# Kernel optimization log

Hardware: AMD Instinct MI355X
Metric: run time of the kernel (lower is better)

The kernel has to match this reference:

```python
import jax, jax.numpy as jnp
import numpy as np

L = 2          # num_layers
B = 64         # batch
T = 256        # seq len (== max_len)
I = 1024       # input_size
H = 1024       # hidden_size
G = 2 * H      # gate size
EPS = 1e-5


def setup_inputs() -> dict:
    key = jax.random.key(0)
    ks = jax.random.split(key, 12)
    stdv = 1.0 / np.sqrt(H)
    u = lambda k, shp: jax.random.uniform(k, shp, jnp.float32, -stdv, stdv)
    return {
        "x": jax.random.normal(ks[0], (B, T, I), jnp.float32),
        "hx": jax.random.normal(ks[1], (L, B, H), jnp.float32),
        "w_ih": u(ks[2], (L, G, I)),
        "w_hh": u(ks[3], (L, G, H)),
        "b_ih": u(ks[4], (L, G)),
        "b_hh": u(ks[5], (L, G)),
        # SeparatedBatchNorm1d affine params: weight ~ U[0,1], bias = 0 (per reset_parameters)
        "bn_i_w": jax.random.uniform(ks[6], (L, G), jnp.float32),
        "bn_i_b": jnp.zeros((L, G), jnp.float32),
        "bn_h_w": jax.random.uniform(ks[7], (L, G), jnp.float32),
        "bn_h_b": jnp.zeros((L, G), jnp.float32),
    }


def _bn(v, w, b):
    # training-mode batch norm over the batch dim (biased variance), affine
    m = jnp.mean(v, axis=0)
    var = jnp.var(v, axis=0)
    return (v - m) * jax.lax.rsqrt(var + EPS) * w + b


def reference(x, hx, w_ih, w_hh, b_ih, b_hh, bn_i_w, bn_i_b, bn_h_w, bn_h_b):
    out = x  # [B, T, I]
    for layer in range(L):
        wih, whh = w_ih[layer], w_hh[layer]
        bih, bhh = b_ih[layer], b_hh[layer]
        iw, ib = bn_i_w[layer], bn_i_b[layer]
        hw, hb = bn_h_w[layer], bn_h_b[layer]

        # precompute input projections + per-step BN outside the recurrence
        def step(h, x_t):
            in_part = _bn(x_t @ wih.T + bih, iw, ib)          # [B, 2H]
            h_part = _bn(h @ whh.T + bhh, hw, hb)             # [B, 2H]
            gates = in_part + h_part
            ug = jax.nn.sigmoid(gates[:, :H])
            og = jax.nn.relu(gates[:, H:])
            h_new = ug * h + (1.0 - ug) * og
            return h_new, h_new

        _, ys = jax.lax.scan(step, hx[layer], jnp.swapaxes(out, 0, 1))  # ys: [T, B, H]
        out = jnp.swapaxes(ys, 0, 1)  # [B, T, H]
    return out
```

## Files before the change

kernel.cpp:

```cpp
#include <hip/hip_runtime.h>
#include <hip/hip_bf16.h>


typedef __attribute__((ext_vector_type(8))) short bf16x8;
typedef __attribute__((ext_vector_type(4))) float f32x4;

__device__ __forceinline__ float wave_sum(float v) {
#pragma unroll
  for (int m = 1; m < 64; m <<= 1) v += __shfl_xor(v, m, 64);
  return v;
}

__device__ __forceinline__ unsigned short f2bf(float f) {
  __hip_bfloat16 h = __float2bfloat16(f);
  return __builtin_bit_cast(unsigned short, h);
}
__device__ __forceinline__ float bf2f(unsigned short u) {
  unsigned int x = ((unsigned int)u) << 16;
  return __builtin_bit_cast(float, x);
}
__device__ __forceinline__ void split2(float v, unsigned short& hi, unsigned short& lo) {
  hi = f2bf(v);
  lo = f2bf(v - bf2f(hi));
}

__global__ __launch_bounds__(256) void wconv(
    const float* __restrict__ w, unsigned short* __restrict__ wh, unsigned short* __restrict__ wl)
{
  int i = ((blockIdx.x << 8) + threadIdx.x) << 3;
#pragma unroll
  for (int j = 0; j < 8; j += 4) {
    float4 a = *(const float4*)(w + i + j);
    ushort4 h, l;
    split2(a.x, h.x, l.x); split2(a.y, h.y, l.y);
    split2(a.z, h.z, l.z); split2(a.w, h.w, l.w);
    *(ushort4*)(wh + i + j) = h;
    *(ushort4*)(wl + i + j) = l;
  }
}

__global__ __launch_bounds__(256) void hinit(
    const float* __restrict__ hx0, unsigned short* __restrict__ hh, unsigned short* __restrict__ hl)
{
  int i = ((blockIdx.x << 8) + threadIdx.x) << 3;
#pragma unroll
  for (int j = 0; j < 8; j += 4) {
    float4 a = *(const float4*)(hx0 + i + j);
    ushort4 h, l;
    split2(a.x, h.x, l.x); split2(a.y, h.y, l.y);
    split2(a.z, h.z, l.z); split2(a.w, h.w, l.w);
    *(ushort4*)(hh + i + j) = h;
    *(ushort4*)(hl + i + j) = l;
  }
}

__global__ __launch_bounds__(256) void proj_gemm(
    const float* __restrict__ in, const float* __restrict__ w,
    float* __restrict__ P, int t0)
{
  __shared__ float As[8][132];
  __shared__ float Bs[8][132];
  const int tid = threadIdx.x;
  const int m0 = blockIdx.y << 7;
  const int n0 = blockIdx.x << 7;
  const int tm = tid >> 4, tn = tid & 15;
  const int lr = tid >> 1;
  const int lk = (tid & 1) << 2;
  const int mA = m0 + lr;
  const int bb = mA & 63;
  const int tg = t0 + (mA >> 6);
  const float* arow = in + ((size_t)bb << 18) + ((size_t)tg << 10) + lk;
  const float* brow = w + ((size_t)(n0 + lr) << 10) + lk;
  float acc[2][2][4][4] = {};
  for (int k0 = 0; k0 < 1024; k0 += 8) {
    float4 av = *(const float4*)(arow + k0);
    float4 bv = *(const float4*)(brow + k0);
    __syncthreads();
    As[lk + 0][lr] = av.x; As[lk + 1][lr] = av.y; As[lk + 2][lr] = av.z; As[lk + 3][lr] = av.w;
    Bs[lk + 0][lr] = bv.x; Bs[lk + 1][lr] = bv.y; Bs[lk + 2][lr] = bv.z; Bs[lk + 3][lr] = bv.w;
    __syncthreads();
#pragma unroll
    for (int kk = 0; kk < 8; ++kk) {
      float4 a0 = *(const float4*)&As[kk][tm << 2];
      float4 a1 = *(const float4*)&As[kk][(tm << 2) + 64];
      float4 b0 = *(const float4*)&Bs[kk][tn << 2];
      float4 b1 = *(const float4*)&Bs[kk][(tn << 2) + 64];
      const float* ap0 = (const float*)&a0;
      const float* ap1 = (const float*)&a1;
      const float* bp0 = (const float*)&b0;
      const float* bp1 = (const float*)&b1;
#pragma unroll
      for (int i = 0; i < 4; ++i)
#pragma unroll
        for (int j = 0; j < 4; ++j) {
          acc[0][0][i][j] = fmaf(ap0[i], bp0[j], acc[0][0][i][j]);
          acc[0][1][i][j] = fmaf(ap0[i], bp1[j], acc[0][1][i][j]);
          acc[1][0][i][j] = fmaf(ap1[i], bp0[j], acc[1][0][i][j]);
          acc[1][1][i][j] = fmaf(ap1[i], bp1[j], acc[1][1][i][j]);
        }
    }
  }
#pragma unroll
  for (int mi = 0; mi < 2; ++mi)
#pragma unroll
    for (int i = 0; i < 4; ++i) {
      int m = m0 + (mi << 6) + (tm << 2) + i;
      float* prow = P + ((size_t)m << 11) + n0 + (tn << 2);
      *(float4*)prow        = make_float4(acc[mi][0][i][0], acc[mi][0][i][1], acc[mi][0][i][2], acc[mi][0][i][3]);
      *(float4*)(prow + 64) = make_float4(acc[mi][1][i][0], acc[mi][1][i][1], acc[mi][1][i][2], acc[mi][1][i][3]);
    }
}

__global__ __launch_bounds__(256) void bn_stats(
    const float* __restrict__ P, const float* __restrict__ iw, const float* __restrict__ ib,
    float* __restrict__ sc, float* __restrict__ sh)
{
  const int t = blockIdx.y;
  const int g = (blockIdx.x << 8) + threadIdx.x;
  const float* col = P + (((size_t)t << 6) << 11) + g;
  float s = 0.f, q = 0.f;
#pragma unroll 8
  for (int b = 0; b < 64; ++b) { float v = col[(size_t)b << 11]; s += v; q = fmaf(v, v, q); }
  float m = s * 0.015625f;
  float var = fmaf(-m, m, q * 0.015625f);
  float scale = iw[g] * rsqrtf(var + 1e-5f);
  sc[(t << 11) + g] = scale;
  sh[(t << 11) + g] = fmaf(-m, scale, ib[g]);
}

__global__ __launch_bounds__(512) void step_mfma(
    const unsigned short* __restrict__ hinh, const unsigned short* __restrict__ hinl,
    unsigned short* __restrict__ houth, unsigned short* __restrict__ houtl,
    const unsigned short* __restrict__ wbh, const unsigned short* __restrict__ wbl,
    const float* __restrict__ P, const float* __restrict__ sc, const float* __restrict__ sh,
    const float* __restrict__ hww, const float* __restrict__ hwb,
    const float* __restrict__ holdbase, long bstride,
    float* __restrict__ out, int t, int tL)
{
  __shared__ float part[8 * 16 * 68];
  __shared__ float lout[64 * 20];
  const int tid = threadIdx.x;
  const int lane = tid & 63;
  const int w = tid >> 6;
  const int tile = w >> 2, kq = w & 3;
  const int c0 = blockIdx.x << 4;
  const int l15 = lane & 15;
  const int koct = (lane >> 4) << 3;

  const int b = lane, cs = w;
  const size_t prow = ((size_t)((tL << 6) + b)) << 11;
  const float pvu0 = P[prow + c0 + cs];
  const float pvu1 = P[prow + c0 + cs + 8];
  const float pvo0 = P[prow + c0 + cs + 1024];
  const float pvo1 = P[prow + c0 + cs + 1032];
  const float hold0 = holdbase[(size_t)b * bstride + c0 + cs];
  const float hold1 = holdbase[(size_t)b * bstride + c0 + cs + 8];

  const int gcol = c0 + l15 + (tile << 10);
  const int kbase = (kq << 8) + koct;
  const size_t woff = ((size_t)gcol << 10) + kbase;
  const size_t aoff = ((size_t)l15 << 10) + kbase;
  const unsigned short* bh = wbh + woff;
  const unsigned short* bl = wbl + woff;
  const unsigned short* ah = hinh + aoff;
  const unsigned short* al = hinl + aoff;
  f32x4 ac0 = {0.f, 0.f, 0.f, 0.f}, ac1 = ac0, ac2 = ac0, ac3 = ac0;
#pragma unroll
  for (int ks = 0; ks < 8; ++ks) {
    const int ko = ks << 5;
    bf16x8 bhv = *(const bf16x8*)(bh + ko);
    bf16x8 blv = *(const bf16x8*)(bl + ko);
    bf16x8 a0h = *(const bf16x8*)(ah + ko);
    bf16x8 a1h = *(const bf16x8*)(ah + ko + (16 << 10));
    bf16x8 a2h = *(const bf16x8*)(ah + ko + (32 << 10));
    bf16x8 a3h = *(const bf16x8*)(ah + ko + (48 << 10));
    bf16x8 a0l = *(const bf16x8*)(al + ko);
    bf16x8 a1l = *(const bf16x8*)(al + ko + (16 << 10));
    bf16x8 a2l = *(const bf16x8*)(al + ko + (32 << 10));
    bf16x8 a3l = *(const bf16x8*)(al + ko + (48 << 10));
    ac0 = __builtin_amdgcn_mfma_f32_16x16x32_bf16(a0h, bhv, ac0, 0, 0, 0);
    ac1 = __builtin_amdgcn_mfma_f32_16x16x32_bf16(a1h, bhv, ac1, 0, 0, 0);
    ac2 = __builtin_amdgcn_mfma_f32_16x16x32_bf16(a2h, bhv, ac2, 0, 0, 0);
    ac3 = __builtin_amdgcn_mfma_f32_16x16x32_bf16(a3h, bhv, ac3, 0, 0, 0);
    ac0 = __builtin_amdgcn_mfma_f32_16x16x32_bf16(a0l, bhv, ac0, 0, 0, 0);
    ac1 = __builtin_amdgcn_mfma_f32_16x16x32_bf16(a1l, bhv, ac1, 0, 0, 0);
    ac2 = __builtin_amdgcn_mfma_f32_16x16x32_bf16(a2l, bhv, ac2, 0, 0, 0);
    ac3 = __builtin_amdgcn_mfma_f32_16x16x32_bf16(a3l, bhv, ac3, 0, 0, 0);
    ac0 = __builtin_amdgcn_mfma_f32_16x16x32_bf16(a0h, blv, ac0, 0, 0, 0);
    ac1 = __builtin_amdgcn_mfma_f32_16x16x32_bf16(a1h, blv, ac1, 0, 0, 0);
    ac2 = __builtin_amdgcn_mfma_f32_16x16x32_bf16(a2h, blv, ac2, 0, 0, 0);
    ac3 = __builtin_amdgcn_mfma_f32_16x16x32_bf16(a3h, blv, ac3, 0, 0, 0);
  }
  {
    float* sp = part + (w * 16 + l15) * 68 + ((lane >> 4) << 2);
    *(f32x4*)(sp +  0) = ac0;
    *(f32x4*)(sp + 16) = ac1;
    *(f32x4*)(sp + 32) = ac2;
    *(f32x4*)(sp + 48) = ac3;
  }
  __syncthreads();

#pragma unroll
  for (int half = 0; half < 2; ++half) {
    const int csub = cs + (half << 3);
    const int gu = c0 + csub;
    float du = part[(0 * 16 + csub) * 68 + b] + part[(1 * 16 + csub) * 68 + b] +
               part[(2 * 16 + csub) * 68 + b] + part[(3 * 16 + csub) * 68 + b];
    float dv = part[(4 * 16 + csub) * 68 + b] + part[(5 * 16 + csub) * 68 + b] +
               part[(6 * 16 + csub) * 68 + b] + part[(7 * 16 + csub) * 68 + b];
    float su = wave_sum(du), qu = wave_sum(du * du);
    float so = wave_sum(dv), qo = wave_sum(dv * dv);
    float mu = su * 0.015625f, vu = fmaf(-mu, mu, qu * 0.015625f);
    float mo = so * 0.015625f, vo = fmaf(-mo, mo, qo * 0.015625f);
    float hpu = (du - mu) * (hww[gu] * rsqrtf(vu + 1e-5f)) + hwb[gu];
    float hpo = (dv - mo) * (hww[gu + 1024] * rsqrtf(vo + 1e-5f)) + hwb[gu + 1024];
    float inu = fmaf(half ? pvu1 : pvu0, sc[(tL << 11) + gu],        sh[(tL << 11) + gu]);
    float ino = fmaf(half ? pvo1 : pvo0, sc[(tL << 11) + gu + 1024], sh[(tL << 11) + gu + 1024]);
    float ug = 1.f / (1.f + expf(-(inu + hpu)));
    float og = fmaxf(ino + hpo, 0.f);
    float hold = half ? hold1 : hold0;
    lout[b * 20 + csub] = fmaf(ug, hold - og, og);
  }
  __syncthreads();

  if (tid < 256) {
    const int b2 = tid >> 2, q = tid & 3;
    float4 v = *(const float4*)&lout[b2 * 20 + (q << 2)];
    *(float4*)(out + (((size_t)(b2 << 8) + t) << 10) + c0 + (q << 2)) = v;
    ushort4 h4, l4;
    split2(v.x, h4.x, l4.x); split2(v.y, h4.y, l4.y);
    split2(v.z, h4.z, l4.z); split2(v.w, h4.w, l4.w);
    *(ushort4*)(houth + ((size_t)b2 << 10) + c0 + (q << 2)) = h4;
    *(ushort4*)(houtl + ((size_t)b2 << 10) + c0 + (q << 2)) = l4;
  }
}

extern "C" void kernel_launch(void* const* d_in, const int* in_sizes, int n_in,
                              void* d_out, int out_size, void* d_ws, size_t ws_size,
                              hipStream_t stream) {
  const float* x   = (const float*)d_in[0];
  const float* hx  = (const float*)d_in[1];
  const float* wih = (const float*)d_in[2];
  const float* whh = (const float*)d_in[3];
  const float* biw = (const float*)d_in[6];
  const float* bib = (const float*)d_in[7];
  const float* bhw = (const float*)d_in[8];
  const float* bhb = (const float*)d_in[9];
  float* out = (float*)d_out;

  const size_t wsf = ws_size / 4;
  const size_t fixedf = 4 * 32768 + 2 * 1048576;
  int TS = 256;
  while (TS > 2) {
    size_t need = fixedf + (size_t)TS * (131072 + 4096);
    if (need <= wsf) break;
    TS >>= 1;
  }
  unsigned short* hAh = (unsigned short*)d_ws;
  unsigned short* hAl = hAh + 65536;
  unsigned short* hBh = hAl + 65536;
  unsigned short* hBl = hBh + 65536;
  unsigned short* wbh = hBl + 65536;
  unsigned short* wbl = wbh + 2097152;
  float* P  = (float*)d_ws + fixedf;
  float* sc = P + (size_t)TS * 131072;
  float* sh = sc + (size_t)TS * 2048;

  for (int layer = 0; layer < 2; ++layer) {
    const float* inp   = layer ? (const float*)out : x;
    const float* wih_l = wih + (size_t)layer * 2048 * 1024;
    const float* whh_l = whh + (size_t)layer * 2048 * 1024;
    const float* biw_l = biw + layer * 2048;
    const float* bib_l = bib + layer * 2048;
    const float* bhw_l = bhw + layer * 2048;
    const float* bhb_l = bhb + layer * 2048;
    const float* hx_l  = hx + (size_t)layer * 65536;

    wconv<<<dim3(1024), 256, 0, stream>>>(whh_l, wbh, wbl);
    hinit<<<dim3(32), 256, 0, stream>>>(hx_l, hAh, hAl);

    for (int t0 = 0; t0 < 256; t0 += TS) {
      proj_gemm<<<dim3(16, TS / 2), 256, 0, stream>>>(inp, wih_l, P, t0);
      bn_stats<<<dim3(8, TS), 256, 0, stream>>>(P, biw_l, bib_l, sc, sh);
      for (int t = t0; t < t0 + TS; ++t) {
        const unsigned short* hinh = (t & 1) ? hBh : hAh;
        const unsigned short* hinl = (t & 1) ? hBl : hAl;
        unsigned short* houth = (t & 1) ? hAh : hBh;
        unsigned short* houtl = (t & 1) ? hAl : hBl;
        const float* holdbase = (t == 0) ? hx_l : (const float*)(out + ((size_t)(t - 1) << 10));
        long bstride = (t == 0) ? 1024 : 262144;
        step_mfma<<<dim3(64), 512, 0, stream>>>(hinh, hinl, houth, houtl, wbh, wbl,
                                                P, sc, sh, bhw_l, bhb_l, holdbase, bstride,
                                                out, t, t - t0);
      }
    }
  }
}
```

Baseline: 13.12 ms.

## Replace per-timestep launches with a persistent cooperative kernel using grid sync

Replaces 256 per-step kernel launches per layer with one cooperative persistent kernel that loops over timesteps and uses grid.sync between steps. The W_hh bf16 hi/lo fragments and the BN affine params are loaded into registers once and reused across all steps. The previous hidden state is also carried in registers instead of being re-read from global memory. This removes launch overhead and repeated weight reloads. The cost is higher register pressure, which may spill under the launch_bounds(512,2) hint, and a grid-wide barrier on every step.

```diff
diff --git a/kernel.cpp b/kernel.cpp
--- a/kernel.cpp
+++ b/kernel.cpp
@@ -1,9 +1,16 @@
 #include <hip/hip_runtime.h>
 #include <hip/hip_bf16.h>
+#include <hip/hip_cooperative_groups.h>
+
+namespace cg = cooperative_groups;
 
 
 typedef __attribute__((ext_vector_type(8))) short bf16x8;
 typedef __attribute__((ext_vector_type(4))) float f32x4;
+
+constexpr size_t H_USH = 64 * 1024;
+constexpr size_t W_USH = 2048 * 1024;
+constexpr size_t FIXED_F = (4 * H_USH + 2 * W_USH) / 2;
 
 __device__ __forceinline__ float wave_sum(float v) {
 #pragma unroll
@@ -128,15 +135,15 @@
   sh[(t << 11) + g] = fmaf(-m, scale, ib[g]);
 }
 
-__global__ __launch_bounds__(512) void step_mfma(
-    const unsigned short* __restrict__ hinh, const unsigned short* __restrict__ hinl,
-    unsigned short* __restrict__ houth, unsigned short* __restrict__ houtl,
+__global__ __launch_bounds__(512, 2) void recur_mfma(
+    unsigned short* __restrict__ hAh, unsigned short* __restrict__ hAl,
+    unsigned short* __restrict__ hBh, unsigned short* __restrict__ hBl,
     const unsigned short* __restrict__ wbh, const unsigned short* __restrict__ wbl,
     const float* __restrict__ P, const float* __restrict__ sc, const float* __restrict__ sh,
     const float* __restrict__ hww, const float* __restrict__ hwb,
-    const float* __restrict__ holdbase, long bstride,
-    float* __restrict__ out, int t, int tL)
-{
+    const float* __restrict__ hx0, float* __restrict__ out, int t0, int TS)
+{
+  cg::grid_group grid = cg::this_grid();
   __shared__ float part[8 * 16 * 68];
   __shared__ float lout[64 * 20];
   const int tid = threadIdx.x;
@@ -147,91 +154,122 @@
   const int l15 = lane & 15;
   const int koct = (lane >> 4) << 3;
 
-  const int b = lane, cs = w;
-  const size_t prow = ((size_t)((tL << 6) + b)) << 11;
-  const float pvu0 = P[prow + c0 + cs];
-  const float pvu1 = P[prow + c0 + cs + 8];
-  const float pvo0 = P[prow + c0 + cs + 1024];
-  const float pvo1 = P[prow + c0 + cs + 1032];
-  const float hold0 = holdbase[(size_t)b * bstride + c0 + cs];
-  const float hold1 = holdbase[(size_t)b * bstride + c0 + cs + 8];
-
   const int gcol = c0 + l15 + (tile << 10);
   const int kbase = (kq << 8) + koct;
   const size_t woff = ((size_t)gcol << 10) + kbase;
-  const size_t aoff = ((size_t)l15 << 10) + kbase;
-  const unsigned short* bh = wbh + woff;
-  const unsigned short* bl = wbl + woff;
-  const unsigned short* ah = hinh + aoff;
-  const unsigned short* al = hinl + aoff;
-  f32x4 ac0 = {0.f, 0.f, 0.f, 0.f}, ac1 = ac0, ac2 = ac0, ac3 = ac0;
+  bf16x8 whr[8], wlr[8];
 #pragma unroll
   for (int ks = 0; ks < 8; ++ks) {
-    const int ko = ks << 5;
-    bf16x8 bhv = *(const bf16x8*)(bh + ko);
-    bf16x8 blv = *(const bf16x8*)(bl + ko);
-    bf16x8 a0h = *(const bf16x8*)(ah + ko);
-    bf16x8 a1h = *(const bf16x8*)(ah + ko + (16 << 10));
-    bf16x8 a2h = *(const bf16x8*)(ah + ko + (32 << 10));
-    bf16x8 a3h = *(const bf16x8*)(ah + ko + (48 << 10));
-    bf16x8 a0l = *(const bf16x8*)(al + ko);
-    bf16x8 a1l = *(const bf16x8*)(al + ko + (16 << 10));
-    bf16x8 a2l = *(const bf16x8*)(al + ko + (32 << 10));
-    bf16x8 a3l = *(const bf16x8*)(al + ko + (48 << 10));
-    ac0 = __builtin_amdgcn_mfma_f32_16x16x32_bf16(a0h, bhv, ac0, 0, 0, 0);
-    ac1 = __builtin_amdgcn_mfma_f32_16x16x32_bf16(a1h, bhv, ac1, 0, 0, 0);
-    ac2 = __builtin_amdgcn_mfma_f32_16x16x32_bf16(a2h, bhv, ac2, 0, 0, 0);
-    ac3 = __builtin_amdgcn_mfma_f32_16x16x32_bf16(a3h, bhv, ac3, 0, 0, 0);
-    ac0 = __builtin_amdgcn_mfma_f32_16x16x32_bf16(a0l, bhv, ac0, 0, 0, 0);
-    ac1 = __builtin_amdgcn_mfma_f32_16x16x32_bf16(a1l, bhv, ac1, 0, 0, 0);
-    ac2 = __builtin_amdgcn_mfma_f32_16x16x32_bf16(a2l, bhv, ac2, 0, 0, 0);
-    ac3 = __builtin_amdgcn_mfma_f32_16x16x32_bf16(a3l, bhv, ac3, 0, 0, 0);
-    ac0 = __builtin_amdgcn_mfma_f32_16x16x32_bf16(a0h, blv, ac0, 0, 0, 0);
-    ac1 = __builtin_amdgcn_mfma_f32_16x16x32_bf16(a1h, blv, ac1, 0, 0, 0);
-    ac2 = __builtin_amdgcn_mfma_f32_16x16x32_bf16(a2h, blv, ac2, 0, 0, 0);
-    ac3 = __builtin_amdgcn_mfma_f32_16x16x32_bf16(a3h, blv, ac3, 0, 0, 0);
-  }
-  {
-    float* sp = part + (w * 16 + l15) * 68 + ((lane >> 4) << 2);
-    *(f32x4*)(sp +  0) = ac0;
-    *(f32x4*)(sp + 16) = ac1;
-    *(f32x4*)(sp + 32) = ac2;
-    *(f32x4*)(sp + 48) = ac3;
-  }
-  __syncthreads();
-
-#pragma unroll
-  for (int half = 0; half < 2; ++half) {
-    const int csub = cs + (half << 3);
-    const int gu = c0 + csub;
-    float du = part[(0 * 16 + csub) * 68 + b] + part[(1 * 16 + csub) * 68 + b] +
-               part[(2 * 16 + csub) * 68 + b] + part[(3 * 16 + csub) * 68 + b];
-    float dv = part[(4 * 16 + csub) * 68 + b] + part[(5 * 16 + csub) * 68 + b] +
-               part[(6 * 16 + csub) * 68 + b] + part[(7 * 16 + csub) * 68 + b];
-    float su = wave_sum(du), qu = wave_sum(du * du);
-    float so = wave_sum(dv), qo = wave_sum(dv * dv);
-    float mu = su * 0.015625f, vu = fmaf(-mu, mu, qu * 0.015625f);
-    float mo = so * 0.015625f, vo = fmaf(-mo, mo, qo * 0.015625f);
-    float hpu = (du - mu) * (hww[gu] * rsqrtf(vu + 1e-5f)) + hwb[gu];
-    float hpo = (dv - mo) * (hww[gu + 1024] * rsqrtf(vo + 1e-5f)) + hwb[gu + 1024];
-    float inu = fmaf(half ? pvu1 : pvu0, sc[(tL << 11) + gu],        sh[(tL << 11) + gu]);
-    float ino = fmaf(half ? pvo1 : pvo0, sc[(tL << 11) + gu + 1024], sh[(tL << 11) + gu + 1024]);
-    float ug = 1.f / (1.f + expf(-(inu + hpu)));
-    float og = fmaxf(ino + hpo, 0.f);
-    float hold = half ? hold1 : hold0;
-    lout[b * 20 + csub] = fmaf(ug, hold - og, og);
-  }
-  __syncthreads();
-
-  if (tid < 256) {
-    const int b2 = tid >> 2, q = tid & 3;
-    float4 v = *(const float4*)&lout[b2 * 20 + (q << 2)];
-    *(float4*)(out + (((size_t)(b2 << 8) + t) << 10) + c0 + (q << 2)) = v;
-    ushort4 h4, l4;
-    split2(v.x, h4.x, l4.x); split2(v.y, h4.y, l4.y);
-    split2(v.z, h4.z, l4.z); split2(v.w, h4.w, l4.w);
-    *(ushort4*)(houth + ((size_t)b2 << 10) + c0 + (q << 2)) = h4;
-    *(ushort4*)(houtl + ((size_t)b2 << 10) + c0 + (q << 2)) = l4;
+    whr[ks] = *(const bf16x8*)(wbh + woff + (ks << 5));
+    wlr[ks] = *(const bf16x8*)(wbl + woff + (ks << 5));
+  }
+
+  const int b = lane, cs = w;
+  const float wwu0 = hww[c0 + cs],        wbu0 = hwb[c0 + cs];
+  const float wwu1 = hww[c0 + cs + 8],    wbu1 = hwb[c0 + cs + 8];
+  const float wwo0 = hww[c0 + cs + 1024], wbo0 = hwb[c0 + cs + 1024];
+  const float wwo1 = hww[c0 + cs + 1032], wbo1 = hwb[c0 + cs + 1032];
+
+  float hold0, hold1;
+  if (t0 == 0) {
+    hold0 = hx0[(b << 10) + c0 + cs];
+    hold1 = hx0[(b << 10) + c0 + cs + 8];
+  } else {
+    const size_t r = (((size_t)(b << 8)) + (t0 - 1)) << 10;
+    hold0 = out[r + c0 + cs];
+    hold1 = out[r + c0 + cs + 8];
+  }
+
+  const size_t aoffbase = ((size_t)l15 << 10) + kbase;
+
+  for (int tL = 0; tL < TS; ++tL) {
+    const int t = t0 + tL;
+    const unsigned short *hh, *hl;
+    unsigned short *oh, *ol;
+    if (t & 1) { hh = hBh; hl = hBl; oh = hAh; ol = hAl; }
+    else       { hh = hAh; hl = hAl; oh = hBh; ol = hBl; }
+
+    const size_t prow = ((size_t)((tL << 6) + b)) << 11;
+    const float pvu0 = P[prow + c0 + cs];
+    const float pvu1 = P[prow + c0 + cs + 8];
+    const float pvo0 = P[prow + c0 + cs + 1024];
+    const float pvo1 = P[prow + c0 + cs + 1032];
+    const float scu0 = sc[(tL << 11) + c0 + cs],        shu0 = sh[(tL << 11) + c0 + cs];
+    const float scu1 = sc[(tL << 11) + c0 + cs + 8],    shu1 = sh[(tL << 11) + c0 + cs + 8];
+    const float sco0 = sc[(tL << 11) + c0 + cs + 1024], sho0 = sh[(tL << 11) + c0 + cs + 1024];
+    const float sco1 = sc[(tL << 11) + c0 + cs + 1032], sho1 = sh[(tL << 11) + c0 + cs + 1032];
+
+    const unsigned short* ah = hh + aoffbase;
+    const unsigned short* al = hl + aoffbase;
+    f32x4 ac0 = {0.f, 0.f, 0.f, 0.f}, ac1 = ac0, ac2 = ac0, ac3 = ac0;
+#pragma unroll
+    for (int ks = 0; ks < 8; ++ks) {
+      const int ko = ks << 5;
+      bf16x8 a0h = *(const bf16x8*)(ah + ko);
+      bf16x8 a1h = *(const bf16x8*)(ah + ko + (16 << 10));
+      bf16x8 a2h = *(const bf16x8*)(ah + ko + (32 << 10));
+      bf16x8 a3h = *(const bf16x8*)(ah + ko + (48 << 10));
+      bf16x8 a0l = *(const bf16x8*)(al + ko);
+      bf16x8 a1l = *(const bf16x8*)(al + ko + (16 << 10));
+      bf16x8 a2l = *(const bf16x8*)(al + ko + (32 << 10));
+      bf16x8 a3l = *(const bf16x8*)(al + ko + (48 << 10));
+      ac0 = __builtin_amdgcn_mfma_f32_16x16x32_bf16(a0h, whr[ks], ac0, 0, 0, 0);
+      ac1 = __builtin_amdgcn_mfma_f32_16x16x32_bf16(a1h, whr[ks], ac1, 0, 0, 0);
+      ac2 = __builtin_amdgcn_mfma_f32_16x16x32_bf16(a2h, whr[ks], ac2, 0, 0, 0);
+      ac3 = __builtin_amdgcn_mfma_f32_16x16x32_bf16(a3h, whr[ks], ac3, 0, 0, 0);
+      ac0 = __builtin_amdgcn_mfma_f32_16x16x32_bf16(a0l, whr[ks], ac0, 0, 0, 0);
+      ac1 = __builtin_amdgcn_mfma_f32_16x16x32_bf16(a1l, whr[ks], ac1, 0, 0, 0);
+      ac2 = __builtin_amdgcn_mfma_f32_16x16x32_bf16(a2l, whr[ks], ac2, 0, 0, 0);
+      ac3 = __builtin_amdgcn_mfma_f32_16x16x32_bf16(a3l, whr[ks], ac3, 0, 0, 0);
+      ac0 = __builtin_amdgcn_mfma_f32_16x16x32_bf16(a0h, wlr[ks], ac0, 0, 0, 0);
+      ac1 = __builtin_amdgcn_mfma_f32_16x16x32_bf16(a1h, wlr[ks], ac1, 0, 0, 0);
+      ac2 = __builtin_amdgcn_mfma_f32_16x16x32_bf16(a2h, wlr[ks], ac2, 0, 0, 0);
+      ac3 = __builtin_amdgcn_mfma_f32_16x16x32_bf16(a3h, wlr[ks], ac3, 0, 0, 0);
+    }
+    {
+      float* sp = part + (w * 16 + l15) * 68 + ((lane >> 4) << 2);
+      *(f32x4*)(sp +  0) = ac0;
+      *(f32x4*)(sp + 16) = ac1;
+      *(f32x4*)(sp + 32) = ac2;
+      *(f32x4*)(sp + 48) = ac3;
+    }
+    __syncthreads();
+
+#pragma unroll
+    for (int half = 0; half < 2; ++half) {
+      const int csub = cs + (half << 3);
+      float du = part[(0 * 16 + csub) * 68 + b] + part[(1 * 16 + csub) * 68 + b] +
+                 part[(2 * 16 + csub) * 68 + b] + part[(3 * 16 + csub) * 68 + b];
+      float dv = part[(4 * 16 + csub) * 68 + b] + part[(5 * 16 + csub) * 68 + b] +
+                 part[(6 * 16 + csub) * 68 + b] + part[(7 * 16 + csub) * 68 + b];
+      float su = wave_sum(du), qu = wave_sum(du * du);
+      float so = wave_sum(dv), qo = wave_sum(dv * dv);
+      float mu = su * 0.015625f, vu = fmaf(-mu, mu, qu * 0.015625f);
+      float mo = so * 0.015625f, vo = fmaf(-mo, mo, qo * 0.015625f);
+      float hpu = (du - mu) * ((half ? wwu1 : wwu0) * rsqrtf(vu + 1e-5f)) + (half ? wbu1 : wbu0);
+      float hpo = (dv - mo) * ((half ? wwo1 : wwo0) * rsqrtf(vo + 1e-5f)) + (half ? wbo1 : wbo0);
+      float inu = fmaf(half ? pvu1 : pvu0, half ? scu1 : scu0, half ? shu1 : shu0);
+      float ino = fmaf(half ? pvo1 : pvo0, half ? sco1 : sco0, half ? sho1 : sho0);
+      float ug = 1.f / (1.f + expf(-(inu + hpu)));
+      float og = fmaxf(ino + hpo, 0.f);
+      float hold = half ? hold1 : hold0;
+      float hnew = fmaf(ug, hold - og, og);
+      if (half) hold1 = hnew; else hold0 = hnew;
+      lout[b * 20 + csub] = hnew;
+    }
+    __syncthreads();
+
+    if (tid < 256) {
+      const int b2 = tid >> 2, q = tid & 3;
+      float4 v = *(const float4*)&lout[b2 * 20 + (q << 2)];
+      *(float4*)(out + (((size_t)(b2 << 8) + t) << 10) + c0 + (q << 2)) = v;
+      ushort4 h4, l4;
+      split2(v.x, h4.x, l4.x); split2(v.y, h4.y, l4.y);
+      split2(v.z, h4.z, l4.z); split2(v.w, h4.w, l4.w);
+      *(ushort4*)(oh + ((size_t)b2 << 10) + c0 + (q << 2)) = h4;
+      *(ushort4*)(ol + ((size_t)b2 << 10) + c0 + (q << 2)) = l4;
+    }
+    grid.sync();
   }
 }
 
@@ -249,20 +287,19 @@
   float* out = (float*)d_out;
 
   const size_t wsf = ws_size / 4;
-  const size_t fixedf = 4 * 32768 + 2 * 1048576;
   int TS = 256;
   while (TS > 2) {
-    size_t need = fixedf + (size_t)TS * (131072 + 4096);
+    size_t need = FIXED_F + (size_t)TS * (131072 + 4096);
     if (need <= wsf) break;
     TS >>= 1;
   }
   unsigned short* hAh = (unsigned short*)d_ws;
-  unsigned short* hAl = hAh + 65536;
-  unsigned short* hBh = hAl + 65536;
-  unsigned short* hBl = hBh + 65536;
-  unsigned short* wbh = hBl + 65536;
-  unsigned short* wbl = wbh + 2097152;
-  float* P  = (float*)d_ws + fixedf;
+  unsigned short* hAl = hAh + H_USH;
+  unsigned short* hBh = hAl + H_USH;
+  unsigned short* hBl = hBh + H_USH;
+  unsigned short* wbh = hBl + H_USH;
+  unsigned short* wbl = wbh + W_USH;
+  float* P  = (float*)d_ws + FIXED_F;
   float* sc = P + (size_t)TS * 131072;
   float* sh = sc + (size_t)TS * 2048;
 
@@ -282,17 +319,12 @@
     for (int t0 = 0; t0 < 256; t0 += TS) {
       proj_gemm<<<dim3(16, TS / 2), 256, 0, stream>>>(inp, wih_l, P, t0);
       bn_stats<<<dim3(8, TS), 256, 0, stream>>>(P, biw_l, bib_l, sc, sh);
-      for (int t = t0; t < t0 + TS; ++t) {
-        const unsigned short* hinh = (t & 1) ? hBh : hAh;
-        const unsigned short* hinl = (t & 1) ? hBl : hAl;
-        unsigned short* houth = (t & 1) ? hAh : hBh;
-        unsigned short* houtl = (t & 1) ? hAl : hBl;
-        const float* holdbase = (t == 0) ? hx_l : (const float*)(out + ((size_t)(t - 1) << 10));
-        long bstride = (t == 0) ? 1024 : 262144;
-        step_mfma<<<dim3(64), 512, 0, stream>>>(hinh, hinl, houth, houtl, wbh, wbl,
-                                                P, sc, sh, bhw_l, bhb_l, holdbase, bstride,
-                                                out, t, t - t0);
-      }
-    }
-  }
-}
+      int ts = TS;
+      void* args[] = { (void*)&hAh, (void*)&hAl, (void*)&hBh, (void*)&hBl,
+                       (void*)&wbh, (void*)&wbl, (void*)&P, (void*)&sc, (void*)&sh,
+                       (void*)&bhw_l, (void*)&bhb_l, (void*)&hx_l, (void*)&out,
+                       (void*)&t0, (void*)&ts };
+      hipLaunchCooperativeKernel((void*)recur_mfma, dim3(64), dim3(512), args, 0, stream);
+    }
+  }
+}
```

New measurement: 15.57 ms. 1.19x slower.
